# Performance work log

Measured on AMD Instinct MI355X. Metric: run time of the kernel, lower is better.

## Reference

```python
import jax, jax.numpy as jnp
import numpy as np

D, N_EXP, N_TOK = 2048, 8, 32768


def setup_inputs() -> dict:
    key = jax.random.key(0)
    k_h, k_eps, k_ww, k_bw, k_wn, k_bn = jax.random.split(key, 6)
    bound = 1.0 / np.sqrt(D)  # nn.Linear default init range
    return {
        "h": jax.random.normal(k_h, (N_TOK, D), dtype=jnp.float32),
        "W_w": jax.random.uniform(k_ww, (D, N_EXP), jnp.float32, -bound, bound),
        "b_w": jax.random.uniform(k_bw, (N_EXP,), jnp.float32, -bound, bound),
        "W_n": jax.random.uniform(k_wn, (D, N_EXP), jnp.float32, -bound, bound),
        "b_n": jax.random.uniform(k_bn, (N_EXP,), jnp.float32, -bound, bound),
        "eps": jax.random.normal(k_eps, (N_TOK, N_EXP), dtype=jnp.float32),
        "top_k": 2,
    }


def reference(h, W_w, b_w, W_n, b_n, eps, top_k):
    # logits = lin_w(h); noise_scale = softplus(lin_noise(h))
    logits = jnp.einsum("td,de->te", h, W_w) + b_w          # [T, E]
    noise = eps * jax.nn.softplus(jnp.einsum("td,de->te", h, W_n) + b_n)
    noisy = logits + noise                                   # [T, E]
    full = jax.nn.softmax(noisy, axis=-1)
    topk_vals, ix = jax.lax.top_k(noisy, top_k)              # [T, k]
    # scatter topk values into -inf tensor == mask non-topk with -inf
    mask = jax.nn.one_hot(ix, noisy.shape[-1], dtype=jnp.bool_).any(axis=-2)  # [T, E]
    sparse = jnp.where(mask, noisy, -jnp.inf)
    return jax.nn.softmax(sparse, axis=-1), ix, full
```

## Files before the change

kernel.cpp:

```cpp
#include <hip/hip_runtime.h>
#include <math.h>

constexpr int D_DIM = 2048;
constexpr int NEXP  = 8;
constexpr int NTOK  = 32768;
constexpr int TT    = 4;
constexpr int KC    = 128;
constexpr int WPB   = 4;

__device__ __forceinline__ float softplus_f(float x) {
    return (x > 20.0f) ? x : log1pf(expf(x));
}

__global__ __launch_bounds__(256, 4)
void noisy_topk_router(const float* __restrict__ h,
                       const float* __restrict__ Ww,
                       const float* __restrict__ bw,
                       const float* __restrict__ Wn,
                       const float* __restrict__ bn,
                       const float* __restrict__ eps,
                       float* __restrict__ out_sparse,
                       float* __restrict__ out_ix,
                       float* __restrict__ out_full)
{
    const int lane = threadIdx.x & 63;
    const int wave = threadIdx.x >> 6;
    const int t0   = (blockIdx.x * WPB + wave) * TT;

    float p[TT * 16];
#pragma unroll
    for (int i = 0; i < TT * 16; ++i) p[i] = 0.0f;

    const float* hbase = h + (size_t)t0 * D_DIM;
    const int lk = lane * 2;

    float2 hv[TT];
#pragma unroll
    for (int t = 0; t < TT; ++t)
        hv[t] = *(const float2*)(hbase + (size_t)t * D_DIM + lk);

#pragma unroll 1
    for (int k0 = 0; k0 < D_DIM; k0 += KC) {
        const int kk = k0 + lk;
        const float4* wwp = (const float4*)(Ww + (size_t)kk * NEXP);
        const float4* wnp = (const float4*)(Wn + (size_t)kk * NEXP);
        float4 ww0 = wwp[0], ww1 = wwp[1], ww2 = wwp[2], ww3 = wwp[3];
        float4 wn0 = wnp[0], wn1 = wnp[1], wn2 = wnp[2], wn3 = wnp[3];

        float2 hvn[TT];
        if (k0 + KC < D_DIM) {
#pragma unroll
            for (int t = 0; t < TT; ++t)
                hvn[t] = *(const float2*)(hbase + (size_t)t * D_DIM + (kk + KC));
        }

        const float wrow0[16] = {ww0.x, ww0.y, ww0.z, ww0.w, ww1.x, ww1.y, ww1.z, ww1.w,
                                 wn0.x, wn0.y, wn0.z, wn0.w, wn1.x, wn1.y, wn1.z, wn1.w};
        const float wrow1[16] = {ww2.x, ww2.y, ww2.z, ww2.w, ww3.x, ww3.y, ww3.z, ww3.w,
                                 wn2.x, wn2.y, wn2.z, wn2.w, wn3.x, wn3.y, wn3.z, wn3.w};

#pragma unroll
        for (int t = 0; t < TT; ++t) {
            const float x0 = hv[t].x, x1 = hv[t].y;
#pragma unroll
            for (int j = 0; j < 16; ++j) {
                p[t * 16 + j] = fmaf(x0, wrow0[j], p[t * 16 + j]);
                p[t * 16 + j] = fmaf(x1, wrow1[j], p[t * 16 + j]);
            }
        }

#pragma unroll
        for (int t = 0; t < TT; ++t) hv[t] = hvn[t];
    }

#pragma unroll
    for (int s = 0; s < 6; ++s) {
        const int m = 1 << s;
        const bool hi = (lane & m) != 0;
        const int n = (TT * 16) >> (s + 1);
#pragma unroll
        for (int j = 0; j < n; ++j) {
            float a  = p[2 * j];
            float b  = p[2 * j + 1];
            float ta = __shfl_xor(a, m, 64);
            float tb = __shfl_xor(b, m, 64);
            p[j] = hi ? (b + tb) : (a + ta);
        }
    }

    const int  e16       = lane & 15;
    const int  eg        = lane & 7;
    const bool noiseLane = (e16 & 8) != 0;
    const int  trow      = lane >> 4;
    const float bias     = noiseLane ? bn[eg] : bw[eg];

    const int tok = t0 + trow;
    const float val = p[0] + bias;
    const float sp  = softplus_f(val);
    const float spN = __shfl_xor(sp, 8, 64);
    const float ev  = eps[(size_t)tok * NEXP + eg];
    const float noisy = val + ev * spN;

    float v0 = noisy; int i0 = eg;
#pragma unroll
    for (int m = 1; m <= 4; m <<= 1) {
        float ov = __shfl_xor(v0, m, 64);
        int   oi = __shfl_xor(i0, m, 64);
        bool take = (ov > v0) || (ov == v0 && oi < i0);
        v0 = take ? ov : v0;
        i0 = take ? oi : i0;
    }
    float v1 = (eg == i0) ? -INFINITY : noisy; int i1 = eg;
#pragma unroll
    for (int m = 1; m <= 4; m <<= 1) {
        float ov = __shfl_xor(v1, m, 64);
        int   oi = __shfl_xor(i1, m, 64);
        bool take = (ov > v1) || (ov == v1 && oi < i1);
        v1 = take ? ov : v1;
        i1 = take ? oi : i1;
    }
    const float ex = expf(noisy - v0);
    float ssum = ex;
#pragma unroll
    for (int m = 1; m <= 4; m <<= 1) ssum += __shfl_xor(ssum, m, 64);
    const float fullv = ex / ssum;
    const float dd  = expf(v1 - v0);
    const float den = 1.0f + dd;
    const float sparsev = (eg == i0) ? (1.0f / den)
                        : (eg == i1) ? (dd / den) : 0.0f;

    if (!noiseLane) {
        out_sparse[(size_t)tok * NEXP + eg] = sparsev;
        out_full  [(size_t)tok * NEXP + eg] = fullv;
        if (eg == 0) {
            out_ix[(size_t)tok * 2]     = (float)i0;
            out_ix[(size_t)tok * 2 + 1] = (float)i1;
        }
    }
}

extern "C" void kernel_launch(void* const* d_in, const int* in_sizes, int n_in,
                              void* d_out, int out_size, void* d_ws, size_t ws_size,
                              hipStream_t stream) {
    const float* h   = (const float*)d_in[0];
    const float* Ww  = (const float*)d_in[1];
    const float* bw  = (const float*)d_in[2];
    const float* Wn  = (const float*)d_in[3];
    const float* bn  = (const float*)d_in[4];
    const float* eps = (const float*)d_in[5];

    float* out_sparse = (float*)d_out;
    float* out_ix     = out_sparse + (size_t)NTOK * NEXP;
    float* out_full   = out_ix + (size_t)NTOK * 2;

    const int grid = NTOK / (TT * WPB);
    noisy_topk_router<<<grid, 256, 0, stream>>>(h, Ww, bw, Wn, bn, eps,
                                                out_sparse, out_ix, out_full);
}
```

Baseline: 390.9 us.

## Split lanes between gate and noise weights, widen h loads to nontemporal float4

Each lane pair now divides the work by weight matrix: even lanes accumulate the eight W_w outputs and odd lanes the eight W_n outputs, each over four consecutive k values. This halves the per-lane accumulator array from 64 to 32 and removes one cross-lane reduction stage. Activations are read as float4 with nontemporal loads so the streaming h data does not pollute the cache. The catch is that both lanes of a pair load the same h vector, and the epilogue lane-to-expert mapping and shuffle masks had to be remapped to match.

```diff
diff --git a/kernel.cpp b/kernel.cpp
--- a/kernel.cpp
+++ b/kernel.cpp
@@ -7,6 +7,8 @@
 constexpr int TT    = 4;
 constexpr int KC    = 128;
 constexpr int WPB   = 4;
+
+typedef float vf4 __attribute__((ext_vector_type(4)));
 
 __device__ __forceinline__ float softplus_f(float x) {
     return (x > 20.0f) ? x : log1pf(expf(x));
@@ -26,46 +28,48 @@
     const int lane = threadIdx.x & 63;
     const int wave = threadIdx.x >> 6;
     const int t0   = (blockIdx.x * WPB + wave) * TT;
+    const int role = lane & 1;
+    const int kg   = lane >> 1;
 
-    float p[TT * 16];
+    float p[TT * 8];
 #pragma unroll
-    for (int i = 0; i < TT * 16; ++i) p[i] = 0.0f;
+    for (int i = 0; i < TT * 8; ++i) p[i] = 0.0f;
 
-    const float* hbase = h + (size_t)t0 * D_DIM;
-    const int lk = lane * 2;
+    const float* __restrict__ Wp = role ? Wn : Ww;
+    const float* hbase = h + (size_t)t0 * D_DIM + 4 * kg;
 
-    float2 hv[TT];
+    vf4 hv[TT];
 #pragma unroll
     for (int t = 0; t < TT; ++t)
-        hv[t] = *(const float2*)(hbase + (size_t)t * D_DIM + lk);
+        hv[t] = __builtin_nontemporal_load((const vf4*)(hbase + (size_t)t * D_DIM));
 
 #pragma unroll 1
     for (int k0 = 0; k0 < D_DIM; k0 += KC) {
-        const int kk = k0 + lk;
-        const float4* wwp = (const float4*)(Ww + (size_t)kk * NEXP);
-        const float4* wnp = (const float4*)(Wn + (size_t)kk * NEXP);
-        float4 ww0 = wwp[0], ww1 = wwp[1], ww2 = wwp[2], ww3 = wwp[3];
-        float4 wn0 = wnp[0], wn1 = wnp[1], wn2 = wnp[2], wn3 = wnp[3];
+        const vf4* wp = (const vf4*)(Wp + (size_t)(k0 + 4 * kg) * NEXP);
+        vf4 w0 = wp[0], w1 = wp[1], w2 = wp[2], w3 = wp[3],
+            w4 = wp[4], w5 = wp[5], w6 = wp[6], w7 = wp[7];
 
-        float2 hvn[TT];
+        vf4 hvn[TT];
         if (k0 + KC < D_DIM) {
 #pragma unroll
             for (int t = 0; t < TT; ++t)
-                hvn[t] = *(const float2*)(hbase + (size_t)t * D_DIM + (kk + KC));
+                hvn[t] = __builtin_nontemporal_load(
+                    (const vf4*)(hbase + (size_t)t * D_DIM + (k0 + KC)));
         }
 
-        const float wrow0[16] = {ww0.x, ww0.y, ww0.z, ww0.w, ww1.x, ww1.y, ww1.z, ww1.w,
-                                 wn0.x, wn0.y, wn0.z, wn0.w, wn1.x, wn1.y, wn1.z, wn1.w};
-        const float wrow1[16] = {ww2.x, ww2.y, ww2.z, ww2.w, ww3.x, ww3.y, ww3.z, ww3.w,
-                                 wn2.x, wn2.y, wn2.z, wn2.w, wn3.x, wn3.y, wn3.z, wn3.w};
+        const float w[32] = {w0[0], w0[1], w0[2], w0[3], w1[0], w1[1], w1[2], w1[3],
+                             w2[0], w2[1], w2[2], w2[3], w3[0], w3[1], w3[2], w3[3],
+                             w4[0], w4[1], w4[2], w4[3], w5[0], w5[1], w5[2], w5[3],
+                             w6[0], w6[1], w6[2], w6[3], w7[0], w7[1], w7[2], w7[3]};
 
 #pragma unroll
         for (int t = 0; t < TT; ++t) {
-            const float x0 = hv[t].x, x1 = hv[t].y;
 #pragma unroll
-            for (int j = 0; j < 16; ++j) {
-                p[t * 16 + j] = fmaf(x0, wrow0[j], p[t * 16 + j]);
-                p[t * 16 + j] = fmaf(x1, wrow1[j], p[t * 16 + j]);
+            for (int d = 0; d < 4; ++d) {
+                const float x = hv[t][d];
+#pragma unroll
+                for (int o = 0; o < 8; ++o)
+                    p[t * 8 + o] = fmaf(x, w[d * 8 + o], p[t * 8 + o]);
             }
         }
 
@@ -74,10 +78,10 @@
     }
 
 #pragma unroll
-    for (int s = 0; s < 6; ++s) {
-        const int m = 1 << s;
+    for (int s = 0; s < 5; ++s) {
+        const int m = 2 << s;
         const bool hi = (lane & m) != 0;
-        const int n = (TT * 16) >> (s + 1);
+        const int n = 32 >> (s + 1);
 #pragma unroll
         for (int j = 0; j < n; ++j) {
             float a  = p[2 * j];
@@ -88,31 +92,29 @@
         }
     }
 
-    const int  e16       = lane & 15;
-    const int  eg        = lane & 7;
-    const bool noiseLane = (e16 & 8) != 0;
-    const int  trow      = lane >> 4;
-    const float bias     = noiseLane ? bn[eg] : bw[eg];
+    const int  o         = (lane >> 1) & 7;
+    const bool noiseLane = (role != 0);
+    const int  tok       = t0 + (lane >> 4);
+    const float bias     = noiseLane ? bn[o] : bw[o];
 
-    const int tok = t0 + trow;
     const float val = p[0] + bias;
     const float sp  = softplus_f(val);
-    const float spN = __shfl_xor(sp, 8, 64);
-    const float ev  = eps[(size_t)tok * NEXP + eg];
+    const float spN = __shfl_xor(sp, 1, 64);
+    const float ev  = eps[(size_t)tok * NEXP + o];
     const float noisy = val + ev * spN;
 
-    float v0 = noisy; int i0 = eg;
+    float v0 = noisy; int i0 = o;
 #pragma unroll
-    for (int m = 1; m <= 4; m <<= 1) {
+    for (int m = 2; m <= 8; m <<= 1) {
         float ov = __shfl_xor(v0, m, 64);
         int   oi = __shfl_xor(i0, m, 64);
         bool take = (ov > v0) || (ov == v0 && oi < i0);
         v0 = take ? ov : v0;
         i0 = take ? oi : i0;
     }
-    float v1 = (eg == i0) ? -INFINITY : noisy; int i1 = eg;
+    float v1 = (o == i0) ? -INFINITY : noisy; int i1 = o;
 #pragma unroll
-    for (int m = 1; m <= 4; m <<= 1) {
+    for (int m = 2; m <= 8; m <<= 1) {
         float ov = __shfl_xor(v1, m, 64);
         int   oi = __shfl_xor(i1, m, 64);
         bool take = (ov > v1) || (ov == v1 && oi < i1);
@@ -122,17 +124,17 @@
     const float ex = expf(noisy - v0);
     float ssum = ex;
 #pragma unroll
-    for (int m = 1; m <= 4; m <<= 1) ssum += __shfl_xor(ssum, m, 64);
+    for (int m = 2; m <= 8; m <<= 1) ssum += __shfl_xor(ssum, m, 64);
     const float fullv = ex / ssum;
     const float dd  = expf(v1 - v0);
     const float den = 1.0f + dd;
-    const float sparsev = (eg == i0) ? (1.0f / den)
-                        : (eg == i1) ? (dd / den) : 0.0f;
+    const float sparsev = (o == i0) ? (1.0f / den)
+                        : (o == i1) ? (dd / den) : 0.0f;
 
     if (!noiseLane) {
-        out_sparse[(size_t)tok * NEXP + eg] = sparsev;
-        out_full  [(size_t)tok * NEXP + eg] = fullv;
-        if (eg == 0) {
+        out_sparse[(size_t)tok * NEXP + o] = sparsev;
+        out_full  [(size_t)tok * NEXP + o] = fullv;
+        if (o == 0) {
             out_ix[(size_t)tok * 2]     = (float)i0;
             out_ix[(size_t)tok * 2 + 1] = (float)i1;
         }
```

After: 432.4 us. +10.6%, slower.
